# Kernel tuning notes

Measured on AMD Instinct MI355X. Metric: run time of the kernel, lower is better.

Reference implementation:

```python
import jax, jax.numpy as jnp
import numpy as np

B, L, D = 16, 2048, 320          # batch, frames, mel_filter_size * mask_size (80*4)
CODE_DIM = 16                     # code_book_size (projection output dim)
NUM_CODES = 8192                  # num_code_books (codebook entries)
N_MASK = (B * L) // 2             # fixed number of masked positions (static for jit)


def setup_inputs() -> dict:
    key = jax.random.key(0)
    k1, k2, k3, k4 = jax.random.split(key, 4)
    input_values = jax.random.normal(k1, (B, L, D), dtype=jnp.float32)
    # mask with exactly N_MASK ones so the gather has a static size
    perm = jax.random.permutation(k2, B * L)
    mask_flat = jnp.zeros((B * L,), jnp.int32).at[perm[:N_MASK]].set(1)
    mask_time_indices = mask_flat.reshape(B, L)
    # xavier_uniform for Linear(D -> CODE_DIM), weight shape (CODE_DIM, D)
    limit = float(np.sqrt(6.0 / (D + CODE_DIM)))
    proj_weight = jax.random.uniform(k3, (CODE_DIM, D), jnp.float32, -limit, limit)
    code_book = jax.random.normal(k4, (NUM_CODES, CODE_DIM), dtype=jnp.float32)
    return {
        "input_values": input_values,
        "mask_time_indices": mask_time_indices,
        "proj_weight": proj_weight,
        "code_book": code_book,
    }


def reference(input_values, mask_time_indices, proj_weight, code_book):
    d = input_values.shape[-1]
    x = input_values.reshape(-1, d)                      # (B*L, D)
    mask = mask_time_indices.reshape(-1)
    idx = jnp.nonzero(mask == 1, size=N_MASK)[0]         # static-size gather of masked rows
    rows = x[idx]                                        # (N, D)
    targets = rows @ proj_weight.T                       # (N, CODE_DIM)
    # ||t - c||_2 via the GEMM expansion ||t||^2 + ||c||^2 - 2 t.c (avoids (N,K,S) blowup)
    t2 = jnp.sum(targets * targets, axis=-1, keepdims=True)       # (N, 1)
    c2 = jnp.sum(code_book * code_book, axis=-1)                  # (K,)
    d2 = t2 + c2[None, :] - 2.0 * (targets @ code_book.T)         # (N, K)
    dist = jnp.sqrt(jnp.maximum(d2, 0.0))
    # torch.argmin with no dim flattens -> scalar index into the (N*K) array
    labels = jnp.argmin(dist)
    return labels
```

## Files before the change

kernel.cpp:

```cpp
#include <hip/hip_runtime.h>
#include <hip/hip_bf16.h>


#define NMASK   16384
#define NROWS   32768
#define D       320
#define CDIM    16
#define NCODES  8192
#define EPS_C   2e-4f
#define EPS_ABS 0.02f

typedef __attribute__((ext_vector_type(8))) short short8;
typedef __attribute__((ext_vector_type(4))) float f32x4;

__device__ inline unsigned int encf(float f) {
  unsigned int u = __float_as_uint(f);
  return (u & 0x80000000u) ? ~u : (u | 0x80000000u);
}
__device__ inline float decf(unsigned int u) {
  unsigned int b = (u & 0x80000000u) ? (u & 0x7fffffffu) : ~u;
  return __uint_as_float(b);
}
__device__ inline unsigned short f2bf(float f) {
  unsigned int u = __float_as_uint(f);
  unsigned int r = u + 0x7fffu + ((u >> 16) & 1u);
  return (unsigned short)(r >> 16);
}
__device__ inline float bf2f(unsigned short h) {
  return __uint_as_float(((unsigned int)h) << 16);
}

__device__ inline void proj_lds(const float* __restrict__ x,
                                const float* __restrict__ Wl,
                                int row, int ch, float pd[16]) {
  const float* xr = x + (size_t)row * D + ch * 4;
  float4 xv[10];
#pragma unroll
  for (int j = 0; j < 10; ++j) xv[j] = *(const float4*)(xr + j * 32);
#pragma unroll
  for (int c = 0; c < 16; ++c) pd[c] = 0.f;
#pragma unroll
  for (int j = 0; j < 10; ++j) {
#pragma unroll
    for (int c = 0; c < 16; ++c) {
      const float4 wv = *(const float4*)&Wl[c * D + j * 32 + ch * 4];
      float acc = fmaf(xv[j].x, wv.x, pd[c]);
      acc = fmaf(xv[j].y, wv.y, acc);
      acc = fmaf(xv[j].z, wv.z, acc);
      pd[c] = fmaf(xv[j].w, wv.w, acc);
    }
  }
#pragma unroll
  for (int c = 0; c < 16; ++c) {
    pd[c] += __shfl_xor(pd[c], 1);
    pd[c] += __shfl_xor(pd[c], 2);
    pd[c] += __shfl_xor(pd[c], 4);
  }
}

__global__ void init_kernel(unsigned int* __restrict__ ctrs,
                            unsigned long long* __restrict__ key) {
  if (threadIdx.x < 4) ctrs[threadIdx.x] = 0u;
  if (threadIdx.x == 4) key[0] = 0xFFFFFFFFFFFFFFFFull;
}

__global__ __launch_bounds__(256) void project_kernel(
    const float* __restrict__ x, const int* __restrict__ mask,
    const float* __restrict__ W, const float* __restrict__ cbk,
    float* __restrict__ c2, unsigned int* __restrict__ cnrm,
    unsigned short* __restrict__ cbf32, unsigned short* __restrict__ tbf32,
    float* __restrict__ t2arr, int* __restrict__ origrow,
    unsigned int* __restrict__ slotctr) {
  __shared__ float Wl[CDIM * D];
  __shared__ unsigned long long mb;
  __shared__ unsigned int wcnt[4], wbase[4];
  int tid = threadIdx.x, bid = (int)blockIdx.x;
  int chunk = bid >> 1, half = bid & 1;
  for (int i = tid; i < (CDIM * D) / 4; i += 256)
    ((float4*)Wl)[i] = ((const float4*)W)[i];
  if (tid < 64) {
    int m = mask[chunk * 64 + tid];
    unsigned long long bal = __ballot(m != 0);
    if (tid == 0) mb = bal;
  }
  __syncthreads();

  if (bid < 512 && tid < 16) {
    int k = bid * 16 + tid;
    const float4* p = (const float4*)(cbk + (long)k * CDIM);
    float s = 0.f; unsigned short chv[16], clv[16];
#pragma unroll
    for (int q = 0; q < 4; ++q) {
      float4 v = p[q];
      s = fmaf(v.x, v.x, s); s = fmaf(v.y, v.y, s);
      s = fmaf(v.z, v.z, s); s = fmaf(v.w, v.w, s);
      float m2[4] = {-2.0f * v.x, -2.0f * v.y, -2.0f * v.z, -2.0f * v.w};
#pragma unroll
      for (int e = 0; e < 4; ++e) {
        unsigned short hi = f2bf(m2[e]);
        chv[q*4+e] = hi;
        clv[q*4+e] = f2bf(m2[e] - bf2f(hi));
      }
    }
    c2[k] = s;
    unsigned short g1 = f2bf(s), g2 = f2bf(s - bf2f(g1));
    cnrm[k] = (unsigned int)g1 | ((unsigned int)g2 << 16);
    uint4 pk0, pk1, pk2, pk3;
    pk0.x = (unsigned int)chv[0]  | ((unsigned int)chv[1]  << 16);
    pk0.y = (unsigned int)chv[2]  | ((unsigned int)chv[3]  << 16);
    pk0.z = (unsigned int)chv[4]  | ((unsigned int)chv[5]  << 16);
    pk0.w = (unsigned int)chv[6]  | ((unsigned int)chv[7]  << 16);
    pk1.x = (unsigned int)chv[8]  | ((unsigned int)chv[9]  << 16);
    pk1.y = (unsigned int)chv[10] | ((unsigned int)chv[11] << 16);
    pk1.z = (unsigned int)chv[12] | ((unsigned int)chv[13] << 16);
    pk1.w = (unsigned int)chv[14] | ((unsigned int)chv[15] << 16);
    pk2.x = (unsigned int)clv[0]  | ((unsigned int)clv[1]  << 16);
    pk2.y = (unsigned int)clv[2]  | ((unsigned int)clv[3]  << 16);
    pk2.z = (unsigned int)clv[4]  | ((unsigned int)clv[5]  << 16);
    pk2.w = (unsigned int)clv[6]  | ((unsigned int)clv[7]  << 16);
    pk3.x = (unsigned int)clv[8]  | ((unsigned int)clv[9]  << 16);
    pk3.y = (unsigned int)clv[10] | ((unsigned int)clv[11] << 16);
    pk3.z = (unsigned int)clv[12] | ((unsigned int)clv[13] << 16);
    pk3.w = (unsigned int)clv[14] | ((unsigned int)clv[15] << 16);
    uint4* dst = (uint4*)(cbf32 + (long)k * 32);
    dst[0] = pk0; dst[1] = pk1; dst[2] = pk2; dst[3] = pk3;
  }

  unsigned long long B0 = mb;
  int r = tid >> 3, ch = tid & 7, lane = tid & 63, w = tid >> 6;
  int p = half * 32 + r;
  int row = chunk * 64 + p;
  int m = (int)((B0 >> p) & 1ull);

  unsigned long long wbal = __ballot(m && ch == 0);
  if (lane == 0) wcnt[w] = (unsigned int)__popcll(wbal);
  __syncthreads();
  if (tid == 0) {
    unsigned int tot = wcnt[0] + wcnt[1] + wcnt[2] + wcnt[3];
    unsigned int b = tot ? atomicAdd(slotctr, tot) : 0u;
    wbase[0] = b;
    wbase[1] = b + wcnt[0];
    wbase[2] = b + wcnt[0] + wcnt[1];
    wbase[3] = b + wcnt[0] + wcnt[1] + wcnt[2];
  }
  __syncthreads();
  if (!m) return;

  float pd[16];
  proj_lds(x, Wl, row, ch, pd);

  if (ch == 0) {
    int slot = (int)wbase[w] + __popcll(wbal & ((1ull << lane) - 1ull));
    float t2 = 0.f;
#pragma unroll
    for (int c = 0; c < 16; ++c) t2 = fmaf(pd[c], pd[c], t2);
    t2arr[slot] = t2;
    origrow[slot] = row;
    unsigned short th[16], tl[16];
#pragma unroll
    for (int c = 0; c < 16; ++c) {
      unsigned short hi = f2bf(pd[c]);
      th[c] = hi;
      tl[c] = f2bf(pd[c] - bf2f(hi));
    }
    uint4 pk0, pk1, pk2, pk3;
    pk0.x = (unsigned int)th[0]  | ((unsigned int)th[1]  << 16);
    pk0.y = (unsigned int)th[2]  | ((unsigned int)th[3]  << 16);
    pk0.z = (unsigned int)th[4]  | ((unsigned int)th[5]  << 16);
    pk0.w = (unsigned int)th[6]  | ((unsigned int)th[7]  << 16);
    pk1.x = (unsigned int)th[8]  | ((unsigned int)th[9]  << 16);
    pk1.y = (unsigned int)th[10] | ((unsigned int)th[11] << 16);
    pk1.z = (unsigned int)th[12] | ((unsigned int)th[13] << 16);
    pk1.w = (unsigned int)th[14] | ((unsigned int)th[15] << 16);
    pk2.x = (unsigned int)tl[0]  | ((unsigned int)tl[1]  << 16);
    pk2.y = (unsigned int)tl[2]  | ((unsigned int)tl[3]  << 16);
    pk2.z = (unsigned int)tl[4]  | ((unsigned int)tl[5]  << 16);
    pk2.w = (unsigned int)tl[6]  | ((unsigned int)tl[7]  << 16);
    pk3.x = (unsigned int)tl[8]  | ((unsigned int)tl[9]  << 16);
    pk3.y = (unsigned int)tl[10] | ((unsigned int)tl[11] << 16);
    pk3.z = (unsigned int)tl[12] | ((unsigned int)tl[13] << 16);
    pk3.w = (unsigned int)tl[14] | ((unsigned int)tl[15] << 16);
    uint4* dst = (uint4*)(tbf32 + (long)slot * 32);
    dst[0] = pk0; dst[1] = pk1; dst[2] = pk2; dst[3] = pk3;
  }
}

__global__ __launch_bounds__(512) void phase1_kernel(
    const unsigned short* __restrict__ tbf32,
    const unsigned short* __restrict__ cbf32,
    const unsigned int* __restrict__ cnrm,
    const float* __restrict__ t2arr,
    unsigned int* __restrict__ rowmin_u) {
  __shared__ unsigned int rml[8 * 65];
  int tid = threadIdx.x;
  int w = tid >> 6, l = tid & 63, lr = l & 15, g = l >> 4;
  int row0 = (int)blockIdx.x * 64;

  for (int i = tid; i < 8 * 65; i += 512) rml[i] = 0xFFFFFFFFu;

  const f32x4 zero = {0.f, 0.f, 0.f, 0.f};
  short8 calA = {0,0,0,0,0,0,0,0}, calB = {0,0,0,0,0,0,0,0};
  if (g == 0) {
    calA[0] = (short)f2bf((float)(lr + 1));
    calB[0] = (short)0x3F80;
  }
  f32x4 cal = __builtin_amdgcn_mfma_f32_16x16x32_bf16(calA, calB, zero, 0, 0, 0);
  int rid[4];
#pragma unroll
  for (int j = 0; j < 4; ++j) {
    int v = (int)(cal[j] + 0.5f) - 1;
    rid[j] = v < 0 ? 0 : (v > 15 ? 15 : v);
  }

  short8 a1[4], a2[4];
  f32x4 rmin[4];
#pragma unroll
  for (int rg = 0; rg < 4; ++rg) {
    int row = row0 + rg * 16 + lr;
    a1[rg] = *(const short8*)(tbf32 + (long)row * 32 + g * 8);
    short8 t = {0,0,0,0,0,0,0,0};
    if (g < 2) {
      t = a1[rg];
    } else if (g == 2) {
      float t2v = t2arr[row];
      unsigned short h1 = f2bf(t2v), h2 = f2bf(t2v - bf2f(h1));
      t[0] = (short)0x3F80; t[1] = (short)0x3F80;
      t[2] = (short)h1;     t[3] = (short)h2;
    }
    a2[rg] = t;
    rmin[rg] = (f32x4){3.4e38f, 3.4e38f, 3.4e38f, 3.4e38f};
  }

  int cbase = w * 1024;
#pragma unroll 2
  for (int t = 0; t < 64; ++t) {
    int code = cbase + t * 16 + lr;
    const unsigned short* cb = cbf32 + (long)code * 32;
    short8 bh = *(const short8*)(cb + (g & 1) * 8);
    short8 b2 = {0,0,0,0,0,0,0,0};
    if (g < 2) {
      b2 = *(const short8*)(cb + 16 + g * 8);
    } else if (g == 2) {
      unsigned int cn = cnrm[code];
      b2[0] = (short)(cn & 0xFFFFu);
      b2[1] = (short)(cn >> 16);
      b2[2] = (short)0x3F80; b2[3] = (short)0x3F80;
    }
#pragma unroll
    for (int rg = 0; rg < 4; ++rg) {
      f32x4 d = __builtin_amdgcn_mfma_f32_16x16x32_bf16(a1[rg], bh, zero, 0, 0, 0);
      d = __builtin_amdgcn_mfma_f32_16x16x32_bf16(a2[rg], b2, d, 0, 0, 0);
#pragma unroll
      for (int j = 0; j < 4; ++j) rmin[rg][j] = fminf(rmin[rg][j], d[j]);
    }
  }
  __syncthreads();
  unsigned int* myw = &rml[w * 65];
#pragma unroll
  for (int rg = 0; rg < 4; ++rg)
#pragma unroll
    for (int j = 0; j < 4; ++j)
      atomicMin(&myw[rg * 16 + rid[j]], encf(rmin[rg][j]));
  __syncthreads();
  if (tid < 64) {
    unsigned int mn = 0xFFFFFFFFu;
#pragma unroll
    for (int ww = 0; ww < 8; ++ww) mn = min(mn, rml[ww * 65 + tid]);
    rowmin_u[row0 + tid] = mn;
  }
}

__global__ __launch_bounds__(1024) void gate_kernel(
    const unsigned int* __restrict__ rowmin_u, const float* __restrict__ t2arr,
    const float* __restrict__ c2,
    unsigned int* __restrict__ candcount, int* __restrict__ candlist) {
  __shared__ float red_f[1024];
  __shared__ unsigned int cnt_s;
  int tid = threadIdx.x;
  float cm = 0.f;
  for (int i = tid; i < NCODES; i += 1024) cm = fmaxf(cm, c2[i]);
  red_f[tid] = cm;
  if (tid == 0) cnt_s = 0u;
  __syncthreads();
  for (int s = 512; s > 0; s >>= 1) {
    if (tid < s) red_f[tid] = fmaxf(red_f[tid], red_f[tid + s]);
    __syncthreads();
  }
  float c2m = red_f[0];
  __syncthreads();
  float Tl = 3.4e38f;
  for (int i = tid; i < NMASK; i += 1024) {
    float a = decf(rowmin_u[i]);
    float e = fmaf(EPS_C, sqrtf(t2arr[i] * c2m), EPS_ABS);
    Tl = fminf(Tl, a + e);
  }
  red_f[tid] = Tl;
  __syncthreads();
  for (int s = 512; s > 0; s >>= 1) {
    if (tid < s) red_f[tid] = fminf(red_f[tid], red_f[tid + s]);
    __syncthreads();
  }
  float T = red_f[0];
  for (int i = tid; i < NMASK; i += 1024) {
    float a = decf(rowmin_u[i]);
    float e = fmaf(EPS_C, sqrtf(t2arr[i] * c2m), EPS_ABS);
    if (!(a - e > T)) {
      unsigned int pos = atomicAdd(&cnt_s, 1u);
      candlist[pos] = i;
    }
  }
  __syncthreads();
  if (tid == 0) candcount[0] = cnt_s;
}

__global__ __launch_bounds__(256) void cproj_kernel(
    const float* __restrict__ x, const float* __restrict__ W,
    const int* __restrict__ origrow, const unsigned int* __restrict__ candcount,
    const int* __restrict__ candlist, float* __restrict__ tgtm) {
  int tid = threadIdx.x, bid = (int)blockIdx.x;
  int nc = (int)candcount[0];
  if (bid * 32 >= nc) return;
  __shared__ float Wl[CDIM * D];
  for (int i = tid; i < (CDIM * D) / 4; i += 256)
    ((float4*)Wl)[i] = ((const float4*)W)[i];
  __syncthreads();
  int idx = bid * 32 + (tid >> 3);
  int ch  = tid & 7;
  if (idx >= nc) return;
  int row = origrow[candlist[idx]];
  float pd[16];
  proj_lds(x, Wl, row, ch, pd);
  if (ch == 0) {
    float* op = tgtm + (long)idx * 16;
#pragma unroll
    for (int c = 0; c < 16; ++c) op[c] = -2.0f * pd[c];
  }
}

__global__ __launch_bounds__(256) void rescore_kernel(
    const float* __restrict__ cbk, const float* __restrict__ c2,
    const float* __restrict__ tgtm, const float* __restrict__ t2arr,
    const int* __restrict__ origrow, const int* __restrict__ mask,
    const unsigned int* __restrict__ candcount, const int* __restrict__ candlist,
    unsigned long long* __restrict__ key, unsigned int* __restrict__ resctr,
    int* __restrict__ out) {
  __shared__ unsigned long long red[256];
  __shared__ int lastf;
  __shared__ unsigned int vlow_s;
  int tid = threadIdx.x, bid = (int)blockIdx.x;
  int nwork = (int)candcount[0] * 8;
  for (int wk = bid; wk < nwork; wk += (int)gridDim.x) {
    int ci = wk >> 3, oct = wk & 7;
    int r = candlist[ci];
    float t2 = t2arr[r];
    int row = origrow[r];
    float tm[16];
    const float4* tp = (const float4*)(tgtm + (long)ci * 16);
#pragma unroll
    for (int q = 0; q < 4; ++q) {
      float4 v = tp[q];
      tm[q*4+0] = v.x; tm[q*4+1] = v.y; tm[q*4+2] = v.z; tm[q*4+3] = v.w;
    }
    float minv = 3.4e38f; int mink = 0;
#pragma unroll 2
    for (int k = 0; k < 4; ++k) {
      int code = oct * 1024 + k * 256 + tid;
      const float4* cp = (const float4*)(cbk + (long)code * CDIM);
      float4 c0 = cp[0], c1 = cp[1], c2v4 = cp[2], c3 = cp[3];
      float acc = fmaf(tm[0],  c0.x, c2[code]);
      acc = fmaf(tm[1],  c0.y, acc);   acc = fmaf(tm[2],  c0.z, acc);
      acc = fmaf(tm[3],  c0.w, acc);   acc = fmaf(tm[4],  c1.x, acc);
      acc = fmaf(tm[5],  c1.y, acc);   acc = fmaf(tm[6],  c1.z, acc);
      acc = fmaf(tm[7],  c1.w, acc);   acc = fmaf(tm[8],  c2v4.x, acc);
      acc = fmaf(tm[9],  c2v4.y, acc); acc = fmaf(tm[10], c2v4.z, acc);
      acc = fmaf(tm[11], c2v4.w, acc); acc = fmaf(tm[12], c3.x, acc);
      acc = fmaf(tm[13], c3.y, acc);   acc = fmaf(tm[14], c3.z, acc);
      acc = fmaf(tm[15], c3.w, acc);
      if (acc < minv) { minv = acc; mink = code; }
    }
    red[tid] = ((unsigned long long)encf(t2 + minv) << 32)
        | (unsigned long long)((unsigned int)row * (unsigned int)NCODES + (unsigned int)mink);
    __syncthreads();
    for (int s = 128; s > 0; s >>= 1) {
      if (tid < s) { if (red[tid + s] < red[tid]) red[tid] = red[tid + s]; }
      __syncthreads();
    }
    if (tid == 0) atomicMin(key, red[0]);
    __syncthreads();
  }
  if (tid == 0) {
    __threadfence();
    lastf = (atomicAdd(resctr, 1u) == (unsigned int)gridDim.x - 1u) ? 1 : 0;
  }
  __syncthreads();
  if (lastf) {
    if (tid == 0)
      vlow_s = (unsigned int)(atomicMin(key, 0xFFFFFFFFFFFFFFFFull) & 0xFFFFFFFFull);
    __syncthreads();
    unsigned int vlow = vlow_s;
    int wrow = (int)(vlow >> 13), wcode = (int)(vlow & 8191u);
    int lo = tid * (NROWS / 256);
    int hi = lo + (NROWS / 256); if (hi > wrow) hi = wrow;
    int cnt = 0;
#pragma unroll 4
    for (int i = lo; i < hi; ++i) cnt += (mask[i] != 0);
    __shared__ int ps[256];
    ps[tid] = cnt;
    __syncthreads();
    for (int s = 128; s > 0; s >>= 1) {
      if (tid < s) ps[tid] += ps[tid + s];
      __syncthreads();
    }
    if (tid == 0) out[0] = ps[0] * NCODES + wcode;
  }
}

extern "C" void kernel_launch(void* const* d_in, const int* in_sizes, int n_in,
                              void* d_out, int out_size, void* d_ws, size_t ws_size,
                              hipStream_t stream) {
  const float* x    = (const float*)d_in[0];
  const int*   mask = (const int*)d_in[1];
  const float* W    = (const float*)d_in[2];
  const float* cbk  = (const float*)d_in[3];
  int* out = (int*)d_out;

  char* ws = (char*)d_ws;
  unsigned int*       ctrs      = (unsigned int*)(ws + 4096);
  unsigned int*       slotctr   = (unsigned int*)(ws + 4096);
  unsigned int*       resctr    = (unsigned int*)(ws + 4100);
  unsigned int*       candcount = (unsigned int*)(ws + 4112);
  unsigned long long* key       = (unsigned long long*)(ws + 8184);
  unsigned int*       rowmin_u  = (unsigned int*)(ws + 8192);
  float*              t2arr     = (float*)(ws + 73728);
  int*                origrow   = (int*)(ws + 139264);
  float*              c2        = (float*)(ws + 204800);
  unsigned int*       cnrm      = (unsigned int*)(ws + 237568);
  unsigned short*     cbf32     = (unsigned short*)(ws + 270336);
  int*                candlist  = (int*)(ws + 270336);
  unsigned short*     tbf32     = (unsigned short*)(ws + 794624);
  float*              tgtm      = (float*)(ws + 794624);

  init_kernel<<<1, 64, 0, stream>>>(ctrs, key);
  project_kernel<<<1024, 256, 0, stream>>>(x, mask, W, cbk, c2, cnrm, cbf32,
                                           tbf32, t2arr, origrow, slotctr);
  phase1_kernel<<<256, 512, 0, stream>>>(tbf32, cbf32, cnrm, t2arr, rowmin_u);
  gate_kernel<<<1, 1024, 0, stream>>>(rowmin_u, t2arr, c2, candcount, candlist);
  cproj_kernel<<<512, 256, 0, stream>>>(x, W, origrow, candcount, candlist, tgtm);
  rescore_kernel<<<512, 256, 0, stream>>>(cbk, c2, tgtm, t2arr, origrow, mask,
                                          candcount, candlist, key, resctr, out);
}
```

Measured before the change: 104.5 us.

## Compact masked rows per block, split phase1 over code segments, fuse gate with candidate projection

The projection kernel now handles 128 rows per block with 256 blocks. It compacts the masked rows into a position list and projects two rows per thread group, so the W reads from LDS are shared across both rows. It also initializes rowmin. Phase1 is split into 2048 smaller blocks, each covering 32 rows times 2048 codes, and merges results through a global atomicMin to get more parallelism. The candidate projection is folded into the single-block gate kernel, which saves one launch but serializes that work onto one block.

```diff
diff --git a/kernel.cpp b/kernel.cpp
--- a/kernel.cpp
+++ b/kernel.cpp
@@ -58,6 +58,43 @@
   }
 }
 
+__device__ inline void store_t(const float pd[16], int slot, int row,
+                               float* __restrict__ t2arr,
+                               int* __restrict__ origrow,
+                               unsigned short* __restrict__ tbf32) {
+  float t2 = 0.f;
+#pragma unroll
+  for (int c = 0; c < 16; ++c) t2 = fmaf(pd[c], pd[c], t2);
+  t2arr[slot] = t2;
+  origrow[slot] = row;
+  unsigned short th[16], tl[16];
+#pragma unroll
+  for (int c = 0; c < 16; ++c) {
+    unsigned short hi = f2bf(pd[c]);
+    th[c] = hi;
+    tl[c] = f2bf(pd[c] - bf2f(hi));
+  }
+  uint4 pk0, pk1, pk2, pk3;
+  pk0.x = (unsigned int)th[0]  | ((unsigned int)th[1]  << 16);
+  pk0.y = (unsigned int)th[2]  | ((unsigned int)th[3]  << 16);
+  pk0.z = (unsigned int)th[4]  | ((unsigned int)th[5]  << 16);
+  pk0.w = (unsigned int)th[6]  | ((unsigned int)th[7]  << 16);
+  pk1.x = (unsigned int)th[8]  | ((unsigned int)th[9]  << 16);
+  pk1.y = (unsigned int)th[10] | ((unsigned int)th[11] << 16);
+  pk1.z = (unsigned int)th[12] | ((unsigned int)th[13] << 16);
+  pk1.w = (unsigned int)th[14] | ((unsigned int)th[15] << 16);
+  pk2.x = (unsigned int)tl[0]  | ((unsigned int)tl[1]  << 16);
+  pk2.y = (unsigned int)tl[2]  | ((unsigned int)tl[3]  << 16);
+  pk2.z = (unsigned int)tl[4]  | ((unsigned int)tl[5]  << 16);
+  pk2.w = (unsigned int)tl[6]  | ((unsigned int)tl[7]  << 16);
+  pk3.x = (unsigned int)tl[8]  | ((unsigned int)tl[9]  << 16);
+  pk3.y = (unsigned int)tl[10] | ((unsigned int)tl[11] << 16);
+  pk3.z = (unsigned int)tl[12] | ((unsigned int)tl[13] << 16);
+  pk3.w = (unsigned int)tl[14] | ((unsigned int)tl[15] << 16);
+  uint4* dst = (uint4*)(tbf32 + (long)slot * 32);
+  dst[0] = pk0; dst[1] = pk1; dst[2] = pk2; dst[3] = pk3;
+}
+
 __global__ void init_kernel(unsigned int* __restrict__ ctrs,
                             unsigned long long* __restrict__ key) {
   if (threadIdx.x < 4) ctrs[threadIdx.x] = 0u;
@@ -70,23 +107,25 @@
     float* __restrict__ c2, unsigned int* __restrict__ cnrm,
     unsigned short* __restrict__ cbf32, unsigned short* __restrict__ tbf32,
     float* __restrict__ t2arr, int* __restrict__ origrow,
-    unsigned int* __restrict__ slotctr) {
+    unsigned int* __restrict__ rowmin_u, unsigned int* __restrict__ slotctr) {
   __shared__ float Wl[CDIM * D];
-  __shared__ unsigned long long mb;
-  __shared__ unsigned int wcnt[4], wbase[4];
+  __shared__ unsigned long long mbs[2];
+  __shared__ int pos[128];
+  __shared__ unsigned int base_s;
   int tid = threadIdx.x, bid = (int)blockIdx.x;
-  int chunk = bid >> 1, half = bid & 1;
+  int rbase = bid * 128;
   for (int i = tid; i < (CDIM * D) / 4; i += 256)
     ((float4*)Wl)[i] = ((const float4*)W)[i];
-  if (tid < 64) {
-    int m = mask[chunk * 64 + tid];
+  if (tid < 128) {
+    int m = mask[rbase + tid];
     unsigned long long bal = __ballot(m != 0);
-    if (tid == 0) mb = bal;
-  }
-  __syncthreads();
-
-  if (bid < 512 && tid < 16) {
-    int k = bid * 16 + tid;
+    if ((tid & 63) == 0) mbs[tid >> 6] = bal;
+  }
+  if (tid < 64) rowmin_u[bid * 64 + tid] = 0xFFFFFFFFu;
+  __syncthreads();
+
+  if (tid < 32) {
+    int k = bid * 32 + tid;
     const float4* p = (const float4*)(cbk + (long)k * CDIM);
     float s = 0.f; unsigned short chv[16], clv[16];
 #pragma unroll
@@ -126,77 +165,89 @@
     dst[0] = pk0; dst[1] = pk1; dst[2] = pk2; dst[3] = pk3;
   }
 
-  unsigned long long B0 = mb;
-  int r = tid >> 3, ch = tid & 7, lane = tid & 63, w = tid >> 6;
-  int p = half * 32 + r;
-  int row = chunk * 64 + p;
-  int m = (int)((B0 >> p) & 1ull);
-
-  unsigned long long wbal = __ballot(m && ch == 0);
-  if (lane == 0) wcnt[w] = (unsigned int)__popcll(wbal);
-  __syncthreads();
-  if (tid == 0) {
-    unsigned int tot = wcnt[0] + wcnt[1] + wcnt[2] + wcnt[3];
-    unsigned int b = tot ? atomicAdd(slotctr, tot) : 0u;
-    wbase[0] = b;
-    wbase[1] = b + wcnt[0];
-    wbase[2] = b + wcnt[0] + wcnt[1];
-    wbase[3] = b + wcnt[0] + wcnt[1] + wcnt[2];
-  }
-  __syncthreads();
-  if (!m) return;
-
-  float pd[16];
-  proj_lds(x, Wl, row, ch, pd);
-
-  if (ch == 0) {
-    int slot = (int)wbase[w] + __popcll(wbal & ((1ull << lane) - 1ull));
-    float t2 = 0.f;
-#pragma unroll
-    for (int c = 0; c < 16; ++c) t2 = fmaf(pd[c], pd[c], t2);
-    t2arr[slot] = t2;
-    origrow[slot] = row;
-    unsigned short th[16], tl[16];
+  unsigned long long B0 = mbs[0], B1 = mbs[1];
+  int cnt0 = __popcll(B0);
+  int cnt  = cnt0 + __popcll(B1);
+  if (tid < 64 && ((B0 >> tid) & 1ull))
+    pos[__popcll(B0 & ((1ull << tid) - 1ull))] = tid;
+  if (tid >= 64 && tid < 128 && ((B1 >> (tid - 64)) & 1ull))
+    pos[cnt0 + __popcll(B1 & ((1ull << (tid - 64)) - 1ull))] = tid;
+  if (tid == 0) base_s = cnt ? atomicAdd(slotctr, (unsigned int)cnt) : 0u;
+  __syncthreads();
+  unsigned int base = base_s;
+
+  int r = tid >> 3, ch = tid & 7;
+  int idx0 = r, idx1 = r + 32;
+  if (idx1 < cnt) {
+    int row0 = rbase + pos[idx0], row1 = rbase + pos[idx1];
+    const float* xr0 = x + (size_t)row0 * D + ch * 4;
+    const float* xr1 = x + (size_t)row1 * D + ch * 4;
+    float4 xv0[10], xv1[10];
+#pragma unroll
+    for (int j = 0; j < 10; ++j) { xv0[j] = *(const float4*)(xr0 + j * 32);
+                                   xv1[j] = *(const float4*)(xr1 + j * 32); }
+    float pd0[16], pd1[16];
+#pragma unroll
+    for (int c = 0; c < 16; ++c) { pd0[c] = 0.f; pd1[c] = 0.f; }
+#pragma unroll
+    for (int j = 0; j < 10; ++j) {
+#pragma unroll
+      for (int c = 0; c < 16; ++c) {
+        const float4 wv = *(const float4*)&Wl[c * D + j * 32 + ch * 4];
+        float a0 = fmaf(xv0[j].x, wv.x, pd0[c]);
+        a0 = fmaf(xv0[j].y, wv.y, a0);
+        a0 = fmaf(xv0[j].z, wv.z, a0);
+        pd0[c] = fmaf(xv0[j].w, wv.w, a0);
+        float a1 = fmaf(xv1[j].x, wv.x, pd1[c]);
+        a1 = fmaf(xv1[j].y, wv.y, a1);
+        a1 = fmaf(xv1[j].z, wv.z, a1);
+        pd1[c] = fmaf(xv1[j].w, wv.w, a1);
+      }
+    }
 #pragma unroll
     for (int c = 0; c < 16; ++c) {
-      unsigned short hi = f2bf(pd[c]);
-      th[c] = hi;
-      tl[c] = f2bf(pd[c] - bf2f(hi));
-    }
-    uint4 pk0, pk1, pk2, pk3;
-    pk0.x = (unsigned int)th[0]  | ((unsigned int)th[1]  << 16);
-    pk0.y = (unsigned int)th[2]  | ((unsigned int)th[3]  << 16);
-    pk0.z = (unsigned int)th[4]  | ((unsigned int)th[5]  << 16);
-    pk0.w = (unsigned int)th[6]  | ((unsigned int)th[7]  << 16);
-    pk1.x = (unsigned int)th[8]  | ((unsigned int)th[9]  << 16);
-    pk1.y = (unsigned int)th[10] | ((unsigned int)th[11] << 16);
-    pk1.z = (unsigned int)th[12] | ((unsigned int)th[13] << 16);
-    pk1.w = (unsigned int)th[14] | ((unsigned int)th[15] << 16);
-    pk2.x = (unsigned int)tl[0]  | ((unsigned int)tl[1]  << 16);
-    pk2.y = (unsigned int)tl[2]  | ((unsigned int)tl[3]  << 16);
-    pk2.z = (unsigned int)tl[4]  | ((unsigned int)tl[5]  << 16);
-    pk2.w = (unsigned int)tl[6]  | ((unsigned int)tl[7]  << 16);
-    pk3.x = (unsigned int)tl[8]  | ((unsigned int)tl[9]  << 16);
-    pk3.y = (unsigned int)tl[10] | ((unsigned int)tl[11] << 16);
-    pk3.z = (unsigned int)tl[12] | ((unsigned int)tl[13] << 16);
-    pk3.w = (unsigned int)tl[14] | ((unsigned int)tl[15] << 16);
-    uint4* dst = (uint4*)(tbf32 + (long)slot * 32);
-    dst[0] = pk0; dst[1] = pk1; dst[2] = pk2; dst[3] = pk3;
-  }
-}
-
-__global__ __launch_bounds__(512) void phase1_kernel(
+      pd0[c] += __shfl_xor(pd0[c], 1);
+      pd0[c] += __shfl_xor(pd0[c], 2);
+      pd0[c] += __shfl_xor(pd0[c], 4);
+    }
+#pragma unroll
+    for (int c = 0; c < 16; ++c) {
+      pd1[c] += __shfl_xor(pd1[c], 1);
+      pd1[c] += __shfl_xor(pd1[c], 2);
+      pd1[c] += __shfl_xor(pd1[c], 4);
+    }
+    if (ch == 0) {
+      store_t(pd0, (int)base + idx0, row0, t2arr, origrow, tbf32);
+      store_t(pd1, (int)base + idx1, row1, t2arr, origrow, tbf32);
+    }
+  } else if (idx0 < cnt) {
+    int row = rbase + pos[idx0];
+    float pd[16];
+    proj_lds(x, Wl, row, ch, pd);
+    if (ch == 0) store_t(pd, (int)base + idx0, row, t2arr, origrow, tbf32);
+  }
+  for (int idx = r + 64; idx < cnt; idx += 32) {
+    int row = rbase + pos[idx];
+    float pd[16];
+    proj_lds(x, Wl, row, ch, pd);
+    if (ch == 0) store_t(pd, (int)base + idx, row, t2arr, origrow, tbf32);
+  }
+}
+
+__global__ __launch_bounds__(256) void phase1_kernel(
     const unsigned short* __restrict__ tbf32,
     const unsigned short* __restrict__ cbf32,
     const unsigned int* __restrict__ cnrm,
     const float* __restrict__ t2arr,
     unsigned int* __restrict__ rowmin_u) {
-  __shared__ unsigned int rml[8 * 65];
+  __shared__ unsigned int rml[4 * 33];
   int tid = threadIdx.x;
   int w = tid >> 6, l = tid & 63, lr = l & 15, g = l >> 4;
-  int row0 = (int)blockIdx.x * 64;
-
-  for (int i = tid; i < 8 * 65; i += 512) rml[i] = 0xFFFFFFFFu;
+  int strip = (int)blockIdx.x >> 2;
+  int seg   = ((int)blockIdx.x & 3) * 4 + w;
+  int row0 = strip * 32;
+
+  for (int i = tid; i < 4 * 33; i += 256) rml[i] = 0xFFFFFFFFu;
 
   const f32x4 zero = {0.f, 0.f, 0.f, 0.f};
   short8 calA = {0,0,0,0,0,0,0,0}, calB = {0,0,0,0,0,0,0,0};
@@ -212,10 +263,10 @@
     rid[j] = v < 0 ? 0 : (v > 15 ? 15 : v);
   }
 
-  short8 a1[4], a2[4];
-  f32x4 rmin[4];
-#pragma unroll
-  for (int rg = 0; rg < 4; ++rg) {
+  short8 a1[2], a2[2];
+  f32x4 rmin[2];
+#pragma unroll
+  for (int rg = 0; rg < 2; ++rg) {
     int row = row0 + rg * 16 + lr;
     a1[rg] = *(const short8*)(tbf32 + (long)row * 32 + g * 8);
     short8 t = {0,0,0,0,0,0,0,0};
@@ -231,10 +282,10 @@
     rmin[rg] = (f32x4){3.4e38f, 3.4e38f, 3.4e38f, 3.4e38f};
   }
 
-  int cbase = w * 1024;
+  int code0 = seg * 512;
 #pragma unroll 2
-  for (int t = 0; t < 64; ++t) {
-    int code = cbase + t * 16 + lr;
+  for (int t = 0; t < 32; ++t) {
+    int code = code0 + t * 16 + lr;
     const unsigned short* cb = cbf32 + (long)code * 32;
     short8 bh = *(const short8*)(cb + (g & 1) * 8);
     short8 b2 = {0,0,0,0,0,0,0,0};
@@ -247,7 +298,7 @@
       b2[2] = (short)0x3F80; b2[3] = (short)0x3F80;
     }
 #pragma unroll
-    for (int rg = 0; rg < 4; ++rg) {
+    for (int rg = 0; rg < 2; ++rg) {
       f32x4 d = __builtin_amdgcn_mfma_f32_16x16x32_bf16(a1[rg], bh, zero, 0, 0, 0);
       d = __builtin_amdgcn_mfma_f32_16x16x32_bf16(a2[rg], b2, d, 0, 0, 0);
 #pragma unroll
@@ -255,28 +306,34 @@
     }
   }
   __syncthreads();
-  unsigned int* myw = &rml[w * 65];
-#pragma unroll
-  for (int rg = 0; rg < 4; ++rg)
+  unsigned int* myw = &rml[w * 33];
+#pragma unroll
+  for (int rg = 0; rg < 2; ++rg)
 #pragma unroll
     for (int j = 0; j < 4; ++j)
       atomicMin(&myw[rg * 16 + rid[j]], encf(rmin[rg][j]));
   __syncthreads();
-  if (tid < 64) {
+  if (tid < 32) {
     unsigned int mn = 0xFFFFFFFFu;
 #pragma unroll
-    for (int ww = 0; ww < 8; ++ww) mn = min(mn, rml[ww * 65 + tid]);
-    rowmin_u[row0 + tid] = mn;
-  }
-}
-
-__global__ __launch_bounds__(1024) void gate_kernel(
-    const unsigned int* __restrict__ rowmin_u, const float* __restrict__ t2arr,
-    const float* __restrict__ c2,
-    unsigned int* __restrict__ candcount, int* __restrict__ candlist) {
+    for (int ww = 0; ww < 4; ++ww) mn = min(mn, rml[ww * 33 + tid]);
+    atomicMin(&rowmin_u[row0 + tid], mn);
+  }
+}
+
+__global__ __launch_bounds__(1024) void gatecp_kernel(
+    const float* __restrict__ x, const float* __restrict__ W,
+    const float* __restrict__ c2, const float* __restrict__ t2arr,
+    const int* __restrict__ origrow, const unsigned int* __restrict__ rowmin_u,
+    unsigned int* __restrict__ candcount, int* __restrict__ candlist,
+    float* __restrict__ tgtm) {
+  __shared__ float Wl[CDIM * D];
   __shared__ float red_f[1024];
   __shared__ unsigned int cnt_s;
   int tid = threadIdx.x;
+
+  for (int i = tid; i < (CDIM * D) / 4; i += 1024)
+    ((float4*)Wl)[i] = ((const float4*)W)[i];
   float cm = 0.f;
   for (int i = tid; i < NCODES; i += 1024) cm = fmaxf(cm, c2[i]);
   red_f[tid] = cm;
@@ -310,30 +367,18 @@
     }
   }
   __syncthreads();
+  int nc = (int)cnt_s;
   if (tid == 0) candcount[0] = cnt_s;
-}
-
-__global__ __launch_bounds__(256) void cproj_kernel(
-    const float* __restrict__ x, const float* __restrict__ W,
-    const int* __restrict__ origrow, const unsigned int* __restrict__ candcount,
-    const int* __restrict__ candlist, float* __restrict__ tgtm) {
-  int tid = threadIdx.x, bid = (int)blockIdx.x;
-  int nc = (int)candcount[0];
-  if (bid * 32 >= nc) return;
-  __shared__ float Wl[CDIM * D];
-  for (int i = tid; i < (CDIM * D) / 4; i += 256)
-    ((float4*)Wl)[i] = ((const float4*)W)[i];
-  __syncthreads();
-  int idx = bid * 32 + (tid >> 3);
-  int ch  = tid & 7;
-  if (idx >= nc) return;
-  int row = origrow[candlist[idx]];
-  float pd[16];
-  proj_lds(x, Wl, row, ch, pd);
-  if (ch == 0) {
-    float* op = tgtm + (long)idx * 16;
-#pragma unroll
-    for (int c = 0; c < 16; ++c) op[c] = -2.0f * pd[c];
+  int grp = tid >> 3, ch = tid & 7;
+  for (int idx = grp; idx < nc; idx += 128) {
+    int row = origrow[candlist[idx]];
+    float pd[16];
+    proj_lds(x, Wl, row, ch, pd);
+    if (ch == 0) {
+      float* op = tgtm + (long)idx * 16;
+#pragma unroll
+      for (int c = 0; c < 16; ++c) op[c] = -2.0f * pd[c];
+    }
   }
 }
 
@@ -441,11 +486,11 @@
   float*              tgtm      = (float*)(ws + 794624);
 
   init_kernel<<<1, 64, 0, stream>>>(ctrs, key);
-  project_kernel<<<1024, 256, 0, stream>>>(x, mask, W, cbk, c2, cnrm, cbf32,
-                                           tbf32, t2arr, origrow, slotctr);
-  phase1_kernel<<<256, 512, 0, stream>>>(tbf32, cbf32, cnrm, t2arr, rowmin_u);
-  gate_kernel<<<1, 1024, 0, stream>>>(rowmin_u, t2arr, c2, candcount, candlist);
-  cproj_kernel<<<512, 256, 0, stream>>>(x, W, origrow, candcount, candlist, tgtm);
+  project_kernel<<<256, 256, 0, stream>>>(x, mask, W, cbk, c2, cnrm, cbf32,
+                                          tbf32, t2arr, origrow, rowmin_u, slotctr);
+  phase1_kernel<<<2048, 256, 0, stream>>>(tbf32, cbf32, cnrm, t2arr, rowmin_u);
+  gatecp_kernel<<<1, 1024, 0, stream>>>(x, W, c2, t2arr, origrow, rowmin_u,
+                                        candcount, candlist, tgtm);
   rescore_kernel<<<512, 256, 0, stream>>>(cbk, c2, tgtm, t2arr, origrow, mask,
                                           candcount, candlist, key, resctr, out);
 }
```

Result: slower. 144.7 us (+38.5%).
